# Kernel tuning notes

Hardware: AMD Instinct MI355X
Metric: run time of the kernel (lower is better)

The kernel has to match this reference:

```python
import jax, jax.numpy as jnp
from jax import lax
import numpy as np

N_PARTICLES = 100000  # number of emitters (state.shape[0])
N_FRAMES = 500


def setup_inputs() -> dict:
    key = jax.random.key(0)
    # one-hot initial state over 2 photophysical states (on/off)
    idx = jax.random.randint(key, (N_PARTICLES,), 0, 2)
    initial = jax.nn.one_hot(idx, 2, dtype=jnp.float32)
    # transition_matrix[0] = identity (stay), transition_matrix[1] = swap (switch)
    transition_matrix = jnp.array(
        [[[1.0, 0.0], [0.0, 1.0]], [[0.0, 1.0], [1.0, 0.0]]], dtype=jnp.float32
    )
    # transition[1][1] from init; chosen so p = initial_trans * randint(1,10) stays in (0,1)
    initial_trans = jnp.array([0.05], dtype=jnp.float32)
    return {
        "initial": initial,
        "transition_matrix": transition_matrix,
        "initial_trans": initial_trans,
        "n_frames": N_FRAMES,
    }


def reference(initial, transition_matrix, initial_trans, n_frames):
    # initial: [N, 2] one-hot float; transition_matrix: [2, 2, 2]; initial_trans: [1]
    N = initial.shape[0]
    base = jax.random.key(42)

    def step(carry, i):
        state, p = carry
        k = jax.random.fold_in(base, i)
        ku, kr = jax.random.split(k)
        # every 100 frames: refresh switching probability p = initial_trans * randint(1, 10)
        r = jax.random.randint(kr, (), 1, 10).astype(jnp.float32)
        p = jnp.where(i % 100 == 0, initial_trans[0] * r, p)
        # Categorical([[0.5, 0.5], [1-p, p]]).sample([N]) -> A in {0,1}^{N,2}
        # row 0 samples 1 w.p. 0.5, row 1 samples 1 w.p. p
        u = jax.random.uniform(ku, (N, 2), dtype=jnp.float32)
        probs1 = jnp.stack([jnp.float32(0.5), p])  # [2] prob of drawing category 1
        A = (u < probs1[None, :]).astype(jnp.float32)  # [N, 2]
        # t = sum(state * A, -1): picks the sample for each particle's current state
        t = jnp.sum(state * A, axis=-1).astype(jnp.int32)  # [N]
        m = transition_matrix[t]  # [N, 2, 2]: identity or swap
        state = jnp.einsum('nc,ncd->nd', state, m)  # [N, 2]
        # original appends np.where(state[:,0]==1)[0]; we return the equivalent
        # fixed-shape indicator state[:, 0] per frame (jit-compatible)
        return (state, p), state[:, 0]

    (_, _), chain = lax.scan(step, (initial, initial_trans[0]), jnp.arange(n_frames))
    return chain  # [n_frames, N]
```

## Files before the change

kernel.cpp:

```cpp
#include <hip/hip_runtime.h>
#include <stdint.h>

__device__ __forceinline__ void tf2x32(uint32_t k0, uint32_t k1,
                                       uint32_t x0, uint32_t x1,
                                       uint32_t& o0, uint32_t& o1) {
  const uint32_t ks2 = k0 ^ k1 ^ 0x1BD11BDAu;
  x0 += k0; x1 += k1;
#define TF_R(r) { x0 += x1; x1 = __builtin_rotateleft32(x1, (r)); x1 ^= x0; }
  TF_R(13) TF_R(15) TF_R(26) TF_R(6)
  x0 += k1; x1 += ks2 + 1u;
  TF_R(17) TF_R(29) TF_R(16) TF_R(24)
  x0 += ks2; x1 += k0 + 2u;
  TF_R(13) TF_R(15) TF_R(26) TF_R(6)
  x0 += k0; x1 += k1 + 3u;
  TF_R(17) TF_R(29) TF_R(16) TF_R(24)
  x0 += k1; x1 += ks2 + 4u;
  TF_R(13) TF_R(15) TF_R(26) TF_R(6)
  x0 += ks2; x1 += k0 + 5u;
#undef TF_R
  o0 = x0; o1 = x1;
}

#define LCHUNK 100
#define LMAX   128
#define F0     8

__global__ __launch_bounds__(256) void hmm_main(
    const float* __restrict__ initial,
    const float* __restrict__ initial_trans,
    float* __restrict__ out,
    uint32_t* __restrict__ ws,
    int N, int nf) {
  __shared__ uint32_t s_ku0[LMAX], s_ku1[LMAX], s_thr[LMAX];
  const int c = blockIdx.y;
  const int c0 = c * LCHUNK;
  const int Leff = min(LCHUNK, nf - c0);
  const float trans = initial_trans[0];

  for (int i = threadIdx.x; i < Leff; i += blockDim.x) {
    const int gi = c0 + i;
    uint32_t f0_, f1_, t0, t1;
    tf2x32(0u, 42u, 0u, (uint32_t)gi, f0_, f1_);
    tf2x32(f0_, f1_, 0u, 0u, t0, t1);
    s_ku0[i] = t0; s_ku1[i] = t1;
    const int jf = gi - (gi % 100);
    uint32_t g0, g1, kr0, kr1, a0, a1, b0, b1, h0, h1, l0, l1;
    tf2x32(0u, 42u, 0u, (uint32_t)jf, g0, g1);
    tf2x32(g0, g1, 0u, 1u, kr0, kr1);
    tf2x32(kr0, kr1, 0u, 0u, a0, a1);
    tf2x32(kr0, kr1, 0u, 1u, b0, b1);
    tf2x32(a0, a1, 0u, 0u, h0, h1);
    tf2x32(b0, b1, 0u, 0u, l0, l1);
    const uint32_t hb = h0 ^ h1, lb = l0 ^ l1;
    const uint32_t off = ((hb % 9u) * 4u + (lb % 9u)) % 9u;
    const float p = trans * (float)(1u + off);
    const uint32_t mant = (uint32_t)ceilf(p * 8388608.0f);
    s_thr[i] = mant << 9;
  }
  __syncthreads();

  const int n = blockIdx.x * blockDim.x + threadIdx.x;
  if (n >= N || Leff <= 0) return;
  const uint32_t twon = 2u * (uint32_t)n;
  float* o = out + (size_t)c0 * N + n;

  uint32_t sA, sB, mf = 0;
  if (c == 0) {
    sA = (initial[2 * n] < 0.5f) ? 1u : 0u;
    sB = sA;
  } else {
    sA = 0u; sB = 1u;
  }

  int f = 0;
  if (c != 0) {
    for (; f < F0 && f < Leff; ++f) {
      const uint32_t ku0 = s_ku0[f], ku1 = s_ku1[f], tp = s_thr[f];
      uint32_t a0, a1, b0, b1;
      tf2x32(ku0, ku1, 0u, twon, a0, a1);
      tf2x32(ku0, ku1, 0u, twon + 1u, b0, b1);
      const uint32_t flip0 = ((a0 ^ a1) < 0x80000000u) ? 1u : 0u;
      const uint32_t flip1 = ((b0 ^ b1) < tp) ? 1u : 0u;
      sA = sA ? (1u ^ flip1) : flip0;
      sB = sB ? (1u ^ flip1) : flip0;
      mf += (sA != sB) ? 1u : 0u;
      o[(size_t)f * N] = sA ? 0.0f : 1.0f;
    }
  }
  for (; f < Leff; ++f) {
    const uint32_t ku0 = s_ku0[f], ku1 = s_ku1[f], tp = s_thr[f];
    if (sA != sB) {
      uint32_t a0, a1, b0, b1;
      tf2x32(ku0, ku1, 0u, twon, a0, a1);
      tf2x32(ku0, ku1, 0u, twon + 1u, b0, b1);
      const uint32_t flip0 = ((a0 ^ a1) < 0x80000000u) ? 1u : 0u;
      const uint32_t flip1 = ((b0 ^ b1) < tp) ? 1u : 0u;
      sA = sA ? (1u ^ flip1) : flip0;
      sB = sB ? (1u ^ flip1) : flip0;
    } else {
      uint32_t a0, a1;
      tf2x32(ku0, ku1, 0u, twon + sA, a0, a1);
      const uint32_t thr = sA ? tp : 0x80000000u;
      sA ^= ((a0 ^ a1) < thr) ? 1u : 0u;
      sB = sA;
    }
    mf += (sA != sB) ? 1u : 0u;
    o[(size_t)f * N] = sA ? 0.0f : 1.0f;
  }
  ws[(size_t)c * N + n] = sA | (sB << 1) | (mf << 2);
}

__global__ __launch_bounds__(256) void hmm_fix(
    const float* __restrict__ initial,
    float* __restrict__ out,
    const uint32_t* __restrict__ ws,
    int N, int C) {
  const int n = blockIdx.x * blockDim.x + threadIdx.x;
  if (n >= N) return;
  uint32_t s = (initial[2 * n] < 0.5f) ? 1u : 0u;
  for (int c = 0; c < C; ++c) {
    const uint32_t w = ws[(size_t)c * N + n];
    if (c > 0 && s == 1u) {
      const int c0 = c * LCHUNK;
      const int mf = (int)(w >> 2);
      for (int f = 0; f < mf; ++f) {
        float* q = out + (size_t)(c0 + f) * N + n;
        *q = 1.0f - *q;
      }
    }
    s = (s == 0u) ? (w & 1u) : ((w >> 1) & 1u);
  }
}

extern "C" void kernel_launch(void* const* d_in, const int* in_sizes, int n_in,
                              void* d_out, int out_size, void* d_ws, size_t ws_size,
                              hipStream_t stream) {
  const float* initial = (const float*)d_in[0];
  const float* initial_trans = (const float*)d_in[2];
  float* out = (float*)d_out;

  const int N = in_sizes[0] / 2;
  const int nf = out_size / N;
  const int C = (nf + LCHUNK - 1) / LCHUNK;
  const int gx = (N + 255) / 256;

  hipLaunchKernelGGL(hmm_main, dim3(gx, C), dim3(256), 0, stream,
                     initial, initial_trans, out, (uint32_t*)d_ws, N, nf);
  hipLaunchKernelGGL(hmm_fix, dim3(gx), dim3(256), 0, stream,
                     initial, out, (uint32_t*)d_ws, N, C);
}
```

Measured before the change: 146.6 us.

## Precompute frame key schedule once and process two particles per thread

Frame keys and thresholds now come from a separate schedule kernel, so each main block no longer rebuilds them redundantly into shared memory. Each main thread now handles two adjacent particles and writes float2 stores. The dual-hypothesis phase ends early once the whole wavefront has merged, using __any, and the rest runs single-state steps without per-frame branching. This adds an extra launch and assumes N is even for the vectorized accesses.

```diff
diff --git a/kernel.cpp b/kernel.cpp
--- a/kernel.cpp
+++ b/kernel.cpp
@@ -22,104 +22,116 @@
 }
 
 #define LCHUNK 100
-#define LMAX   128
 #define F0     8
+
+__global__ __launch_bounds__(256) void hmm_sched(
+    const float* __restrict__ initial_trans,
+    uint4* __restrict__ sched, int nf) {
+  const int gi = blockIdx.x * blockDim.x + threadIdx.x;
+  if (gi >= nf) return;
+  const float trans = initial_trans[0];
+  uint32_t f0_, f1_, t0, t1;
+  tf2x32(0u, 42u, 0u, (uint32_t)gi, f0_, f1_);
+  tf2x32(f0_, f1_, 0u, 0u, t0, t1);
+  const int jf = gi - (gi % 100);
+  uint32_t g0, g1, kr0, kr1, a0, a1, b0, b1, h0, h1, l0, l1;
+  tf2x32(0u, 42u, 0u, (uint32_t)jf, g0, g1);
+  tf2x32(g0, g1, 0u, 1u, kr0, kr1);
+  tf2x32(kr0, kr1, 0u, 0u, a0, a1);
+  tf2x32(kr0, kr1, 0u, 1u, b0, b1);
+  tf2x32(a0, a1, 0u, 0u, h0, h1);
+  tf2x32(b0, b1, 0u, 0u, l0, l1);
+  const uint32_t hb = h0 ^ h1, lb = l0 ^ l1;
+  const uint32_t off = ((hb % 9u) * 4u + (lb % 9u)) % 9u;
+  const float p = trans * (float)(1u + off);
+  const uint32_t mant = (uint32_t)ceilf(p * 8388608.0f);
+  sched[gi] = make_uint4(t0, t1, mant << 9, 0u);
+}
+
+__device__ __forceinline__ uint32_t bothstep(uint32_t k0, uint32_t k1,
+                                             uint32_t tp, uint32_t twon,
+                                             uint32_t& sA, uint32_t& sB) {
+  uint32_t a0, a1, b0, b1;
+  tf2x32(k0, k1, 0u, twon, a0, a1);
+  tf2x32(k0, k1, 0u, twon + 1u, b0, b1);
+  const uint32_t flip0 = ((a0 ^ a1) < 0x80000000u) ? 1u : 0u;
+  const uint32_t flip1 = ((b0 ^ b1) < tp) ? 1u : 0u;
+  sA = sA ? (1u ^ flip1) : flip0;
+  sB = sB ? (1u ^ flip1) : flip0;
+  return (sA != sB) ? 1u : 0u;
+}
+
+__device__ __forceinline__ void mstep(uint32_t k0, uint32_t k1, uint32_t tp,
+                                      uint32_t twon, uint32_t& s) {
+  uint32_t a0, a1;
+  tf2x32(k0, k1, 0u, twon + s, a0, a1);
+  const uint32_t thr = s ? tp : 0x80000000u;
+  s ^= ((a0 ^ a1) < thr) ? 1u : 0u;
+}
 
 __global__ __launch_bounds__(256) void hmm_main(
     const float* __restrict__ initial,
-    const float* __restrict__ initial_trans,
+    const uint4* __restrict__ sched,
     float* __restrict__ out,
-    uint32_t* __restrict__ ws,
+    uint32_t* __restrict__ fin,
     int N, int nf) {
-  __shared__ uint32_t s_ku0[LMAX], s_ku1[LMAX], s_thr[LMAX];
+  const int t = blockIdx.x * blockDim.x + threadIdx.x;
+  const int n0 = 2 * t;
+  if (n0 >= N) return;
   const int c = blockIdx.y;
   const int c0 = c * LCHUNK;
   const int Leff = min(LCHUNK, nf - c0);
-  const float trans = initial_trans[0];
+  if (Leff <= 0) return;
 
-  for (int i = threadIdx.x; i < Leff; i += blockDim.x) {
-    const int gi = c0 + i;
-    uint32_t f0_, f1_, t0, t1;
-    tf2x32(0u, 42u, 0u, (uint32_t)gi, f0_, f1_);
-    tf2x32(f0_, f1_, 0u, 0u, t0, t1);
-    s_ku0[i] = t0; s_ku1[i] = t1;
-    const int jf = gi - (gi % 100);
-    uint32_t g0, g1, kr0, kr1, a0, a1, b0, b1, h0, h1, l0, l1;
-    tf2x32(0u, 42u, 0u, (uint32_t)jf, g0, g1);
-    tf2x32(g0, g1, 0u, 1u, kr0, kr1);
-    tf2x32(kr0, kr1, 0u, 0u, a0, a1);
-    tf2x32(kr0, kr1, 0u, 1u, b0, b1);
-    tf2x32(a0, a1, 0u, 0u, h0, h1);
-    tf2x32(b0, b1, 0u, 0u, l0, l1);
-    const uint32_t hb = h0 ^ h1, lb = l0 ^ l1;
-    const uint32_t off = ((hb % 9u) * 4u + (lb % 9u)) % 9u;
-    const float p = trans * (float)(1u + off);
-    const uint32_t mant = (uint32_t)ceilf(p * 8388608.0f);
-    s_thr[i] = mant << 9;
-  }
-  __syncthreads();
+  const uint4* __restrict__ sch = sched + c0;
+  const uint32_t twon0 = 2u * (uint32_t)n0;
+  const uint32_t twon1 = twon0 + 2u;
+  float2* o = (float2*)(out + (size_t)c0 * N + n0);
+  const int ostr = N >> 1;
 
-  const int n = blockIdx.x * blockDim.x + threadIdx.x;
-  if (n >= N || Leff <= 0) return;
-  const uint32_t twon = 2u * (uint32_t)n;
-  float* o = out + (size_t)c0 * N + n;
+  uint32_t s0A, s0B, s1A, s1B, mf0 = 0, mf1 = 0;
+  int f = 0;
 
-  uint32_t sA, sB, mf = 0;
   if (c == 0) {
-    sA = (initial[2 * n] < 0.5f) ? 1u : 0u;
-    sB = sA;
+    const float4 iv = *(const float4*)(initial + 2 * n0);
+    s0A = (iv.x < 0.5f) ? 1u : 0u;  s0B = s0A;
+    s1A = (iv.z < 0.5f) ? 1u : 0u;  s1B = s1A;
   } else {
-    sA = 0u; sB = 1u;
-  }
-
-  int f = 0;
-  if (c != 0) {
-    for (; f < F0 && f < Leff; ++f) {
-      const uint32_t ku0 = s_ku0[f], ku1 = s_ku1[f], tp = s_thr[f];
-      uint32_t a0, a1, b0, b1;
-      tf2x32(ku0, ku1, 0u, twon, a0, a1);
-      tf2x32(ku0, ku1, 0u, twon + 1u, b0, b1);
-      const uint32_t flip0 = ((a0 ^ a1) < 0x80000000u) ? 1u : 0u;
-      const uint32_t flip1 = ((b0 ^ b1) < tp) ? 1u : 0u;
-      sA = sA ? (1u ^ flip1) : flip0;
-      sB = sB ? (1u ^ flip1) : flip0;
-      mf += (sA != sB) ? 1u : 0u;
-      o[(size_t)f * N] = sA ? 0.0f : 1.0f;
+    s0A = 0u; s0B = 1u; s1A = 0u; s1B = 1u;
+    uint32_t d = 1u;
+    for (; f < Leff; ++f) {
+      if (f >= F0 && !__any((int)d)) break;
+      const uint4 sc = sch[f];
+      const uint32_t d0 = bothstep(sc.x, sc.y, sc.z, twon0, s0A, s0B);
+      const uint32_t d1 = bothstep(sc.x, sc.y, sc.z, twon1, s1A, s1B);
+      mf0 += d0; mf1 += d1; d = d0 | d1;
+      *o = make_float2(s0A ? 0.0f : 1.0f, s1A ? 0.0f : 1.0f);
+      o += ostr;
     }
   }
+  const int fm = f;
   for (; f < Leff; ++f) {
-    const uint32_t ku0 = s_ku0[f], ku1 = s_ku1[f], tp = s_thr[f];
-    if (sA != sB) {
-      uint32_t a0, a1, b0, b1;
-      tf2x32(ku0, ku1, 0u, twon, a0, a1);
-      tf2x32(ku0, ku1, 0u, twon + 1u, b0, b1);
-      const uint32_t flip0 = ((a0 ^ a1) < 0x80000000u) ? 1u : 0u;
-      const uint32_t flip1 = ((b0 ^ b1) < tp) ? 1u : 0u;
-      sA = sA ? (1u ^ flip1) : flip0;
-      sB = sB ? (1u ^ flip1) : flip0;
-    } else {
-      uint32_t a0, a1;
-      tf2x32(ku0, ku1, 0u, twon + sA, a0, a1);
-      const uint32_t thr = sA ? tp : 0x80000000u;
-      sA ^= ((a0 ^ a1) < thr) ? 1u : 0u;
-      sB = sA;
-    }
-    mf += (sA != sB) ? 1u : 0u;
-    o[(size_t)f * N] = sA ? 0.0f : 1.0f;
+    const uint4 sc = sch[f];
+    mstep(sc.x, sc.y, sc.z, twon0, s0A);
+    mstep(sc.x, sc.y, sc.z, twon1, s1A);
+    *o = make_float2(s0A ? 0.0f : 1.0f, s1A ? 0.0f : 1.0f);
+    o += ostr;
   }
-  ws[(size_t)c * N + n] = sA | (sB << 1) | (mf << 2);
+  if (fm < Leff) { s0B = s0A; s1B = s1A; }
+  *(uint2*)(fin + (size_t)c * N + n0) =
+      make_uint2(s0A | (s0B << 1) | (mf0 << 2), s1A | (s1B << 1) | (mf1 << 2));
 }
 
 __global__ __launch_bounds__(256) void hmm_fix(
     const float* __restrict__ initial,
     float* __restrict__ out,
-    const uint32_t* __restrict__ ws,
+    const uint32_t* __restrict__ fin,
     int N, int C) {
   const int n = blockIdx.x * blockDim.x + threadIdx.x;
   if (n >= N) return;
   uint32_t s = (initial[2 * n] < 0.5f) ? 1u : 0u;
   for (int c = 0; c < C; ++c) {
-    const uint32_t w = ws[(size_t)c * N + n];
+    const uint32_t w = fin[(size_t)c * N + n];
     if (c > 0 && s == 1u) {
       const int c0 = c * LCHUNK;
       const int mf = (int)(w >> 2);
@@ -142,10 +154,16 @@
   const int N = in_sizes[0] / 2;
   const int nf = out_size / N;
   const int C = (nf + LCHUNK - 1) / LCHUNK;
-  const int gx = (N + 255) / 256;
 
+  uint4* sched = (uint4*)d_ws;
+  const size_t finoff = (((size_t)nf * 16) + 511) & ~(size_t)511;
+  uint32_t* fin = (uint32_t*)((char*)d_ws + finoff);
+
+  hipLaunchKernelGGL(hmm_sched, dim3((nf + 255) / 256), dim3(256), 0, stream,
+                     initial_trans, sched, nf);
+  const int gx = (N / 2 + 255) / 256;
   hipLaunchKernelGGL(hmm_main, dim3(gx, C), dim3(256), 0, stream,
-                     initial, initial_trans, out, (uint32_t*)d_ws, N, nf);
-  hipLaunchKernelGGL(hmm_fix, dim3(gx), dim3(256), 0, stream,
-                     initial, out, (uint32_t*)d_ws, N, C);
+                     initial, sched, out, fin, N, nf);
+  hipLaunchKernelGGL(hmm_fix, dim3((N + 255) / 256), dim3(256), 0, stream,
+                     initial, out, fin, N, C);
 }
```

Result: faster. 135.6 us (-7.5%).
